# Kernel optimization log

Measured on AMD Instinct MI355X. Metric: run time of the kernel, lower is better.

The kernel has to match this reference:

```python
import jax, jax.numpy as jnp
import numpy as np

E_DIM = 64
N_EMBED = 8192

def setup_inputs() -> dict:
    key = jax.random.key(0)
    k1, k2 = jax.random.split(key)
    x = jax.random.normal(k1, (16, E_DIM, 32, 32), dtype=jnp.float32)   # [B, e_dim, H, W]
    embed = jax.random.normal(k2, (E_DIM, N_EMBED), dtype=jnp.float32)  # codebook [e_dim, n_embed]
    return {"x": x, "embed": embed}

def reference(x, embed):
    e_dim, n_embed = embed.shape
    # NCHW -> NHWC
    xp = jnp.transpose(x, (0, 2, 3, 1))              # [B, H, W, e_dim]
    flat = xp.reshape(-1, e_dim)                     # [N, e_dim]
    # squared-distance expansion: ||f||^2 - 2 f.E + ||e||^2  -> [N, n_embed]
    distance = (jnp.sum(flat * flat, axis=1, keepdims=True)
                - 2.0 * flat @ embed
                + jnp.sum(embed * embed, axis=0, keepdims=True))
    embed_idx = jnp.argmax(-distance, axis=1)        # [N] nearest code ids
    embed_idx = embed_idx.reshape(xp.shape[:-1])     # [B, H, W]
    # gather codes: embedding table is embed.T -> [n_embed, e_dim]
    quantize = jnp.take(embed.T, embed_idx, axis=0)  # [B, H, W, e_dim]
    return quantize
```

## Files before the change

kernel.cpp:

```cpp
#include <hip/hip_runtime.h>


typedef __attribute__((ext_vector_type(8))) __bf16 bf16x8;
typedef __attribute__((ext_vector_type(4))) float f32x4;
typedef unsigned int u32;
typedef unsigned long long u64;

union frag_cast { f32x4 f; bf16x8 b; };
__device__ __forceinline__ bf16x8 as_bf16x8(f32x4 v) { frag_cast u; u.f = v; return u.b; }

#define N_ROWS  16384
#define E_DIM   64
#define N_EMBED 8192
#define NCHUNK  16
#define COLS_PER_BLOCK (N_EMBED / NCHUNK)
#define N_ST (COLS_PER_BLOCK / 64)
#define ROWS_PER_BLOCK 512
#define N_ROWBLK (N_ROWS / ROWS_PER_BLOCK)
#define NT 8
#define MARGIN_THR 2e-3f

#define WS_AH   0u
#define WS_AL   (2u << 20)
#define WS_B    (4u << 20)
#define WS_ET   (6u << 20)
#define WS_BIAS (8u << 20)
#define WS_PB1  (WS_BIAS + (64u << 10))
#define WS_PI1  (WS_PB1 + (1u << 20))
#define WS_PB2  (WS_PI1 + (1u << 20))
#define WS_FIDX (WS_PB2 + (1u << 20))
#define WS_FLAG (WS_FIDX + (64u << 10))
#define WS_CNT  (WS_FLAG + (64u << 10))
#define WS_FKEY (WS_CNT + (4u << 10))

__device__ __forceinline__ u32 f32_key(float s) {
    u32 u = __float_as_uint(s);
    return (u & 0x80000000u) ? ~u : (u | 0x80000000u);
}

__device__ __forceinline__ void async16(const void* g, void* l) {
    __builtin_amdgcn_global_load_lds(
        (const __attribute__((address_space(1))) void*)g,
        (__attribute__((address_space(3))) void*)l, 16, 0, 0);
}

__global__ __launch_bounds__(256) void prep(
        const float* __restrict__ x, const float* __restrict__ embed, char* ws) {
    __shared__ float tile[64][65];
    __bf16* Ah = (__bf16*)(ws + WS_AH);
    __bf16* Al = (__bf16*)(ws + WS_AL);
    float*  eT = (float*)(ws + WS_ET);
    float*  bias = (float*)(ws + WS_BIAS);
    const int t = threadIdx.x;
    const int blk = blockIdx.x;

    if (blk < 256) {
        const int b = blk >> 4, p0 = (blk & 15) * 64;
        {
            const int c = t >> 2, seg = (t & 3) * 16;
            const float* src = x + b * 65536 + c * 1024 + p0 + seg;
#pragma unroll
            for (int i = 0; i < 16; ++i) tile[c][seg + i] = src[i];
        }
        __syncthreads();
        const int p = t >> 2, cq = (t & 3) * 16;
        const long row = b * 1024 + p0 + p;
        bf16x8 vh0, vh1, vl0, vl1;
#pragma unroll
        for (int i = 0; i < 16; ++i) {
            float f = tile[cq + i][p];
            __bf16 h = (__bf16)f;
            __bf16 l = (__bf16)(f - (float)h);
            if (i < 8) { vh0[i] = h; vl0[i] = l; }
            else       { vh1[i - 8] = h; vl1[i - 8] = l; }
        }
        *(bf16x8*)(Ah + row * 64 + cq) = vh0;
        *(bf16x8*)(Ah + row * 64 + cq + 8) = vh1;
        *(bf16x8*)(Al + row * 64 + cq) = vl0;
        *(bf16x8*)(Al + row * 64 + cq + 8) = vl1;
    } else {
        if (blk == 256 && t == 0) *(int*)(ws + WS_CNT) = 0;
        const int g = blk - 256;
        const int jbase = g * 64;
        char* Bg = ws + WS_B + (size_t)g * 16384;
        {
            const int c = t >> 2, seg = (t & 3) * 16;
            const float* src = embed + c * N_EMBED + jbase + seg;
#pragma unroll
            for (int i = 0; i < 16; ++i) tile[c][seg + i] = src[i];
        }
        __syncthreads();
        if (t < 64) {
            float s = 0.f;
#pragma unroll
            for (int c = 0; c < 64; ++c) { float v = tile[c][t]; s = fmaf(v, v, s); }
            bias[jbase + t] = -0.5f * s;
        }
        const int jl = t >> 2, cq = (t & 3) * 16;
        bf16x8 vh0, vh1, vl0, vl1;
#pragma unroll
        for (int i = 0; i < 16; ++i) {
            float f = tile[cq + i][jl];
            eT[(long)(jbase + jl) * 64 + cq + i] = f;
            __bf16 h = (__bf16)f;
            __bf16 l = (__bf16)(f - (float)h);
            if (i < 8) { vh0[i] = h; vl0[i] = l; }
            else       { vh1[i - 8] = h; vl1[i - 8] = l; }
        }
        const int k0 = (cq >> 3), sw = jl & 7;
        __bf16* hi = (__bf16*)Bg + jl * 64;
        __bf16* lo = (__bf16*)(Bg + 8192) + jl * 64;
        *(bf16x8*)(hi + ((k0 ^ sw) * 8))       = vh0;
        *(bf16x8*)(hi + (((k0 + 1) ^ sw) * 8)) = vh1;
        *(bf16x8*)(lo + ((k0 ^ sw) * 8))       = vl0;
        *(bf16x8*)(lo + (((k0 + 1) ^ sw) * 8)) = vl1;
    }
}

__global__ __launch_bounds__(256, 2) void qdist(const char* __restrict__ ws_c, char* __restrict__ ws) {
    __shared__ __align__(16) char smem[2][16384];
    __shared__ __align__(16) float biasLds[512];
    const __bf16* Ah = (const __bf16*)(ws_c + WS_AH);
    const __bf16* Al = (const __bf16*)(ws_c + WS_AL);
    const char* Bws = ws_c + WS_B;
    const float* biasg = (const float*)(ws_c + WS_BIAS);
    float* pb1 = (float*)(ws + WS_PB1);
    int*   pi1 = (int*)(ws + WS_PI1);
    float* pb2 = (float*)(ws + WS_PB2);

    const int t = threadIdx.x;
    const int wv = t >> 6, lane = t & 63, ln = lane & 15, q = lane >> 4;
    const int rb = blockIdx.x >> 4, chunk = blockIdx.x & 15;
    const int row0 = rb * ROWS_PER_BLOCK;
    const int col0 = chunk * COLS_PER_BLOCK;
    const int g0 = col0 >> 6;

    f32x4 pfh[NT][2], pfl[NT][2];
#pragma unroll
    for (int nt = 0; nt < NT; ++nt) {
        long row = row0 + wv * 128 + nt * 16 + ln;
        long base = row * 64 + q * 8;
        pfh[nt][0] = *(const f32x4*)(Ah + base);
        pfh[nt][1] = *(const f32x4*)(Ah + base + 32);
        pfl[nt][0] = *(const f32x4*)(Al + base);
        pfl[nt][1] = *(const f32x4*)(Al + base + 32);
    }
    asm volatile("" :
        "+v"(pfh[0][0]), "+v"(pfh[0][1]), "+v"(pfh[1][0]), "+v"(pfh[1][1]),
        "+v"(pfh[2][0]), "+v"(pfh[2][1]), "+v"(pfh[3][0]), "+v"(pfh[3][1]),
        "+v"(pfh[4][0]), "+v"(pfh[4][1]), "+v"(pfh[5][0]), "+v"(pfh[5][1]),
        "+v"(pfh[6][0]), "+v"(pfh[6][1]), "+v"(pfh[7][0]), "+v"(pfh[7][1]));
    asm volatile("" :
        "+v"(pfl[0][0]), "+v"(pfl[0][1]), "+v"(pfl[1][0]), "+v"(pfl[1][1]),
        "+v"(pfl[2][0]), "+v"(pfl[2][1]), "+v"(pfl[3][0]), "+v"(pfl[3][1]),
        "+v"(pfl[4][0]), "+v"(pfl[4][1]), "+v"(pfl[5][0]), "+v"(pfl[5][1]),
        "+v"(pfl[6][0]), "+v"(pfl[6][1]), "+v"(pfl[7][0]), "+v"(pfl[7][1]));

    float b1[NT], b2[NT]; int iq[NT];
#pragma unroll
    for (int k = 0; k < NT; ++k) { b1[k] = -3.4e38f; b2[k] = -3.4e38f; iq[k] = 0; }

    const int s7 = ln & 7;
    const int rdbase = ln * 128 + ((q ^ s7) << 4);

    auto issue = [&](int st) {
        const char* src = Bws + (size_t)(g0 + st) * 16384;
        char* dst = smem[st & 1];
#pragma unroll
        for (int s = 0; s < 4; ++s)
            async16(src + s * 4096 + wv * 1024 + lane * 16,
                    dst + s * 4096 + wv * 1024);
    };

    if (wv < 2)
        async16((const char*)(biasg + col0) + wv * 1024 + lane * 16,
                (char*)biasLds + wv * 1024);
    issue(0);
    asm volatile("s_waitcnt vmcnt(0)" ::: "memory");
    __builtin_amdgcn_s_barrier();
    __builtin_amdgcn_sched_barrier(0);

    for (int st = 0; st < N_ST; ++st) {
        if (st + 1 < N_ST) {
            issue(st + 1);
            asm volatile("s_waitcnt vmcnt(4)" ::: "memory");
        } else {
            asm volatile("s_waitcnt vmcnt(0)" ::: "memory");
        }
        __builtin_amdgcn_s_barrier();
        __builtin_amdgcn_sched_barrier(0);

        const char* buf = smem[st & 1];
#pragma unroll
        for (int ct = 0; ct < 4; ++ct) {
            const int boff = ct * 2048 + rdbase;
            bf16x8 ah0 = *(const bf16x8*)(buf + boff);
            bf16x8 ah1 = *(const bf16x8*)(buf + (boff ^ 64));
            bf16x8 al0 = *(const bf16x8*)(buf + 8192 + boff);
            bf16x8 al1 = *(const bf16x8*)(buf + 8192 + (boff ^ 64));
            f32x4 bv = *(const f32x4*)(biasLds + st * 64 + ct * 16 + q * 4);
            const int jq = col0 + st * 64 + ct * 16 + q * 4;
            __builtin_amdgcn_sched_barrier(0);
            __builtin_amdgcn_s_barrier();
            asm volatile("s_waitcnt lgkmcnt(0)" ::: "memory");
            __builtin_amdgcn_sched_barrier(0);
            __builtin_amdgcn_s_setprio(1);
#pragma unroll
            for (int nt = 0; nt < NT; ++nt) {
                f32x4 acc = __builtin_amdgcn_mfma_f32_16x16x32_bf16(al0, as_bf16x8(pfh[nt][0]), bv, 0, 0, 0);
                acc = __builtin_amdgcn_mfma_f32_16x16x32_bf16(al1, as_bf16x8(pfh[nt][1]), acc, 0, 0, 0);
                acc = __builtin_amdgcn_mfma_f32_16x16x32_bf16(ah0, as_bf16x8(pfl[nt][0]), acc, 0, 0, 0);
                acc = __builtin_amdgcn_mfma_f32_16x16x32_bf16(ah1, as_bf16x8(pfl[nt][1]), acc, 0, 0, 0);
                acc = __builtin_amdgcn_mfma_f32_16x16x32_bf16(ah0, as_bf16x8(pfh[nt][0]), acc, 0, 0, 0);
                acc = __builtin_amdgcn_mfma_f32_16x16x32_bf16(ah1, as_bf16x8(pfh[nt][1]), acc, 0, 0, 0);
                float mx = fmaxf(fmaxf(acc[0], acc[1]), fmaxf(acc[2], acc[3]));
                b2[nt] = fmaxf(b2[nt], fminf(b1[nt], mx));
                bool gt = mx > b1[nt];
                b1[nt] = fmaxf(b1[nt], mx);
                iq[nt] = gt ? jq : iq[nt];
            }
            __builtin_amdgcn_s_setprio(0);
            __builtin_amdgcn_sched_barrier(0);
            __builtin_amdgcn_s_barrier();
            __builtin_amdgcn_sched_barrier(0);
        }
    }

#pragma unroll
    for (int m = 16; m < 64; m <<= 1) {
#pragma unroll
        for (int nt = 0; nt < NT; ++nt) {
            float o1 = __shfl_xor(b1[nt], m);
            int   oi = __shfl_xor(iq[nt], m);
            float o2 = __shfl_xor(b2[nt], m);
            b2[nt] = fmaxf(fmaxf(fminf(b1[nt], o1), o2), b2[nt]);
            bool take = (o1 > b1[nt]) || (o1 == b1[nt] && oi < iq[nt]);
            if (take) { b1[nt] = o1; iq[nt] = oi; }
        }
    }
    if (q == 0) {
#pragma unroll
        for (int nt = 0; nt < NT; ++nt) {
            int pixel = row0 + wv * 128 + nt * 16 + ln;
            int o = chunk * N_ROWS + pixel;
            pb1[o] = b1[nt];
            pi1[o] = iq[nt];
            pb2[o] = b2[nt];
        }
    }
}

__global__ __launch_bounds__(64) void reduce_rows(const float* __restrict__ x, char* ws,
                                                  float* __restrict__ out) {
    const float* pb1 = (const float*)(ws + WS_PB1);
    const int*   pi1 = (const int*)(ws + WS_PI1);
    const float* pb2 = (const float*)(ws + WS_PB2);
    const float* eT = (const float*)(ws + WS_ET);
    const float* bias = (const float*)(ws + WS_BIAS);
    int* flags = (int*)(ws + WS_FLAG);
    int* cnt = (int*)(ws + WS_CNT);
    u64* fkey = (u64*)(ws + WS_FKEY);
    const int row = blockIdx.x * 64 + threadIdx.x;

    float b1 = pb1[row]; int iq = pi1[row]; float b2 = pb2[row];
#pragma unroll
    for (int ch = 1; ch < NCHUNK; ++ch) {
        float o1 = pb1[ch * N_ROWS + row];
        int   oi = pi1[ch * N_ROWS + row];
        float o2 = pb2[ch * N_ROWS + row];
        b2 = fmaxf(fmaxf(fminf(b1, o1), o2), b2);
        if (o1 > b1 || (o1 == b1 && oi < iq)) { b1 = o1; iq = oi; }
    }

    if (b1 - b2 < MARGIN_THR) {
        fkey[row] = 0ull;
        flags[atomicAdd(cnt, 1)] = row;
    } else {
        float xr[64];
        const float* xb = x + (row >> 10) * 65536 + (row & 1023);
#pragma unroll
        for (int c = 0; c < 64; ++c) xr[c] = xb[c * 1024];
        float best = -3.4e38f; int bi = iq;
#pragma unroll
        for (int cc = 0; cc < 4; ++cc) {
            const int j = iq + cc;
            const float* e = eT + j * 64;
            float s = bias[j];
#pragma unroll
            for (int c = 0; c < 64; ++c) s = fmaf(xr[c], e[c], s);
            if (s > best) { best = s; bi = j; }
        }
        const f32x4* src = (const f32x4*)(eT + (size_t)bi * 64);
        f32x4* dst = (f32x4*)(out + (size_t)row * 64);
#pragma unroll
        for (int v = 0; v < 16; ++v) dst[v] = src[v];
    }
}

__global__ __launch_bounds__(256) void recheck(const float* __restrict__ x, char* ws) {
    __shared__ float fl[64];
    __shared__ u64 red[256];
    const float* eT = (const float*)(ws + WS_ET);
    const float* bias = (const float*)(ws + WS_BIAS);
    const int* flags = (const int*)(ws + WS_FLAG);
    const int n = *(const int*)(ws + WS_CNT);
    u64* fkey = (u64*)(ws + WS_FKEY);
    const int t = threadIdx.x;
    const int seg = blockIdx.x & 31;
    const int rstep = gridDim.x >> 5;
    const int j = seg * 256 + t;

    for (int rowi = blockIdx.x >> 5; rowi < n; rowi += rstep) {
        const int row = flags[rowi];
        __syncthreads();
        if (t < 64) fl[t] = x[(row >> 10) * 65536 + t * 1024 + (row & 1023)];
        __syncthreads();
        float xr[64];
#pragma unroll
        for (int c = 0; c < 64; ++c) xr[c] = fl[c];

        const f32x4* e = (const f32x4*)(eT + (size_t)j * 64);
        f32x4 a0 = {0.f, 0.f, 0.f, 0.f}, a1 = a0, a2 = a0, a3 = a0;
#pragma unroll
        for (int v = 0; v < 4; ++v) {
            f32x4 e0 = e[v * 4 + 0], e1 = e[v * 4 + 1];
            f32x4 e2 = e[v * 4 + 2], e3 = e[v * 4 + 3];
#pragma unroll
            for (int k = 0; k < 4; ++k) {
                a0[k] = fmaf(xr[v * 16 + k],      e0[k], a0[k]);
                a1[k] = fmaf(xr[v * 16 + 4 + k],  e1[k], a1[k]);
                a2[k] = fmaf(xr[v * 16 + 8 + k],  e2[k], a2[k]);
                a3[k] = fmaf(xr[v * 16 + 12 + k], e3[k], a3[k]);
            }
        }
        f32x4 a01 = a0 + a1, a23 = a2 + a3;
        f32x4 as = a01 + a23;
        float s = bias[j] + ((as[0] + as[1]) + (as[2] + as[3]));

        red[t] = ((u64)f32_key(s) << 32) | (u32)(~(u32)j);
        __syncthreads();
        for (int off = 128; off; off >>= 1) {
            if (t < off) { u64 o = red[t + off]; if (o > red[t]) red[t] = o; }
            __syncthreads();
        }
        if (t == 0) atomicMax(&fkey[row], red[0]);
        __syncthreads();
    }
}

__global__ __launch_bounds__(256) void gather_fix(const char* __restrict__ ws,
                                                  float* __restrict__ out) {
    const int n = *(const int*)(ws + WS_CNT);
    const int* flags = (const int*)(ws + WS_FLAG);
    const u64* fkey = (const u64*)(ws + WS_FKEY);
    const float* eT = (const float*)(ws + WS_ET);
    const int sub = threadIdx.x >> 6, c = threadIdx.x & 63;
    for (int i = blockIdx.x * 4 + sub; i < n; i += gridDim.x * 4) {
        const int row = flags[i];
        const int idx = (int)(~(u32)(fkey[row] & 0xffffffffull));
        out[(size_t)row * 64 + c] = eT[(size_t)idx * 64 + c];
    }
}

extern "C" void kernel_launch(void* const* d_in, const int* in_sizes, int n_in,
                              void* d_out, int out_size, void* d_ws, size_t ws_size,
                              hipStream_t stream) {
    const float* x     = (const float*)d_in[0];
    const float* embed = (const float*)d_in[1];
    float* out = (float*)d_out;
    char* ws = (char*)d_ws;

    prep<<<384, 256, 0, stream>>>(x, embed, ws);
    qdist<<<N_ROWBLK * NCHUNK, 256, 0, stream>>>(ws, ws);
    reduce_rows<<<N_ROWS / 64, 64, 0, stream>>>(x, ws, out);
    recheck<<<2048, 256, 0, stream>>>(x, ws);
    gather_fix<<<64, 256, 0, stream>>>(ws, out);
}
```

Baseline: 131.0 us.

## Use single fp16 MFMA pass with error-bounded margin and per-chunk recheck queue

Replaces the split bf16 hi/lo three-product MFMA distance computation with a single fp16 product, halving the codebook and activation staging and cutting MFMA work by a factor of three. The fixed margin threshold becomes a per-row error bound derived from the feature norm and the max codebook norm. Rows within the bound are rechecked exactly, but only in the 512-column chunks whose candidate scores are near the best, fed through a work queue. The qdist loop also drops its per-tile barriers in favour of one sync per stage. Risks include fp16 range/precision issues and a larger recheck set if the bound is loose.

```diff
diff --git a/kernel.cpp b/kernel.cpp
--- a/kernel.cpp
+++ b/kernel.cpp
@@ -1,13 +1,11 @@
 #include <hip/hip_runtime.h>
 
 
-typedef __attribute__((ext_vector_type(8))) __bf16 bf16x8;
+typedef _Float16 f16;
+typedef __attribute__((ext_vector_type(8))) _Float16 f16x8;
 typedef __attribute__((ext_vector_type(4))) float f32x4;
 typedef unsigned int u32;
 typedef unsigned long long u64;
-
-union frag_cast { f32x4 f; bf16x8 b; };
-__device__ __forceinline__ bf16x8 as_bf16x8(f32x4 v) { frag_cast u; u.f = v; return u.b; }
 
 #define N_ROWS  16384
 #define E_DIM   64
@@ -18,20 +16,19 @@
 #define ROWS_PER_BLOCK 512
 #define N_ROWBLK (N_ROWS / ROWS_PER_BLOCK)
 #define NT 8
-#define MARGIN_THR 2e-3f
 
 #define WS_AH   0u
-#define WS_AL   (2u << 20)
-#define WS_B    (4u << 20)
-#define WS_ET   (6u << 20)
-#define WS_BIAS (8u << 20)
-#define WS_PB1  (WS_BIAS + (64u << 10))
+#define WS_B    (2u << 20)
+#define WS_ET   (3u << 20)
+#define WS_BIAS (5u << 20)
+#define WS_CNT  (WS_BIAS + (32u << 10))
+#define WS_GN   (WS_CNT + 16u)
+#define WS_PB1  (WS_CNT + (4u << 10))
 #define WS_PI1  (WS_PB1 + (1u << 20))
 #define WS_PB2  (WS_PI1 + (1u << 20))
-#define WS_FIDX (WS_PB2 + (1u << 20))
-#define WS_FLAG (WS_FIDX + (64u << 10))
-#define WS_CNT  (WS_FLAG + (64u << 10))
-#define WS_FKEY (WS_CNT + (4u << 10))
+#define WS_FLAG (WS_PB2 + (1u << 20))
+#define WS_FKEY (WS_FLAG + (64u << 10))
+#define WS_QUEUE (WS_FKEY + (128u << 10))
 
 __device__ __forceinline__ u32 f32_key(float s) {
     u32 u = __float_as_uint(s);
@@ -47,10 +44,10 @@
 __global__ __launch_bounds__(256) void prep(
         const float* __restrict__ x, const float* __restrict__ embed, char* ws) {
     __shared__ float tile[64][65];
-    __bf16* Ah = (__bf16*)(ws + WS_AH);
-    __bf16* Al = (__bf16*)(ws + WS_AL);
+    f16* Ah = (f16*)(ws + WS_AH);
     float*  eT = (float*)(ws + WS_ET);
     float*  bias = (float*)(ws + WS_BIAS);
+    float*  gn = (float*)(ws + WS_GN);
     const int t = threadIdx.x;
     const int blk = blockIdx.x;
 
@@ -65,24 +62,23 @@
         __syncthreads();
         const int p = t >> 2, cq = (t & 3) * 16;
         const long row = b * 1024 + p0 + p;
-        bf16x8 vh0, vh1, vl0, vl1;
+        f16x8 v0, v1;
 #pragma unroll
         for (int i = 0; i < 16; ++i) {
             float f = tile[cq + i][p];
-            __bf16 h = (__bf16)f;
-            __bf16 l = (__bf16)(f - (float)h);
-            if (i < 8) { vh0[i] = h; vl0[i] = l; }
-            else       { vh1[i - 8] = h; vl1[i - 8] = l; }
-        }
-        *(bf16x8*)(Ah + row * 64 + cq) = vh0;
-        *(bf16x8*)(Ah + row * 64 + cq + 8) = vh1;
-        *(bf16x8*)(Al + row * 64 + cq) = vl0;
-        *(bf16x8*)(Al + row * 64 + cq + 8) = vl1;
+            if (i < 8) v0[i] = (f16)f;
+            else       v1[i - 8] = (f16)f;
+        }
+        *(f16x8*)(Ah + row * 64 + cq) = v0;
+        *(f16x8*)(Ah + row * 64 + cq + 8) = v1;
     } else {
-        if (blk == 256 && t == 0) *(int*)(ws + WS_CNT) = 0;
+        if (blk == 256 && t == 0) {
+            ((int*)(ws + WS_CNT))[0] = 0;
+            ((int*)(ws + WS_CNT))[1] = 0;
+        }
         const int g = blk - 256;
         const int jbase = g * 64;
-        char* Bg = ws + WS_B + (size_t)g * 16384;
+        f16* Bg = (f16*)(ws + WS_B) + (size_t)g * 4096;
         {
             const int c = t >> 2, seg = (t & 3) * 16;
             const float* src = embed + c * N_EMBED + jbase + seg;
@@ -95,33 +91,31 @@
 #pragma unroll
             for (int c = 0; c < 64; ++c) { float v = tile[c][t]; s = fmaf(v, v, s); }
             bias[jbase + t] = -0.5f * s;
+            float m = s;
+#pragma unroll
+            for (int off = 1; off < 64; off <<= 1) m = fmaxf(m, __shfl_xor(m, off));
+            if (t == 0) gn[g] = m;
         }
         const int jl = t >> 2, cq = (t & 3) * 16;
-        bf16x8 vh0, vh1, vl0, vl1;
+        f16x8 v0, v1;
 #pragma unroll
         for (int i = 0; i < 16; ++i) {
             float f = tile[cq + i][jl];
             eT[(long)(jbase + jl) * 64 + cq + i] = f;
-            __bf16 h = (__bf16)f;
-            __bf16 l = (__bf16)(f - (float)h);
-            if (i < 8) { vh0[i] = h; vl0[i] = l; }
-            else       { vh1[i - 8] = h; vl1[i - 8] = l; }
+            if (i < 8) v0[i] = (f16)f;
+            else       v1[i - 8] = (f16)f;
         }
         const int k0 = (cq >> 3), sw = jl & 7;
-        __bf16* hi = (__bf16*)Bg + jl * 64;
-        __bf16* lo = (__bf16*)(Bg + 8192) + jl * 64;
-        *(bf16x8*)(hi + ((k0 ^ sw) * 8))       = vh0;
-        *(bf16x8*)(hi + (((k0 + 1) ^ sw) * 8)) = vh1;
-        *(bf16x8*)(lo + ((k0 ^ sw) * 8))       = vl0;
-        *(bf16x8*)(lo + (((k0 + 1) ^ sw) * 8)) = vl1;
+        f16* hi = Bg + jl * 64;
+        *(f16x8*)(hi + ((k0 ^ sw) * 8))       = v0;
+        *(f16x8*)(hi + (((k0 + 1) ^ sw) * 8)) = v1;
     }
 }
 
 __global__ __launch_bounds__(256, 2) void qdist(const char* __restrict__ ws_c, char* __restrict__ ws) {
-    __shared__ __align__(16) char smem[2][16384];
+    __shared__ __align__(16) char smem[2][8192];
     __shared__ __align__(16) float biasLds[512];
-    const __bf16* Ah = (const __bf16*)(ws_c + WS_AH);
-    const __bf16* Al = (const __bf16*)(ws_c + WS_AL);
+    const f16* Ah = (const f16*)(ws_c + WS_AH);
     const char* Bws = ws_c + WS_B;
     const float* biasg = (const float*)(ws_c + WS_BIAS);
     float* pb1 = (float*)(ws + WS_PB1);
@@ -135,26 +129,19 @@
     const int col0 = chunk * COLS_PER_BLOCK;
     const int g0 = col0 >> 6;
 
-    f32x4 pfh[NT][2], pfl[NT][2];
+    f16x8 pf[NT][2];
 #pragma unroll
     for (int nt = 0; nt < NT; ++nt) {
         long row = row0 + wv * 128 + nt * 16 + ln;
         long base = row * 64 + q * 8;
-        pfh[nt][0] = *(const f32x4*)(Ah + base);
-        pfh[nt][1] = *(const f32x4*)(Ah + base + 32);
-        pfl[nt][0] = *(const f32x4*)(Al + base);
-        pfl[nt][1] = *(const f32x4*)(Al + base + 32);
+        pf[nt][0] = *(const f16x8*)(Ah + base);
+        pf[nt][1] = *(const f16x8*)(Ah + base + 32);
     }
     asm volatile("" :
-        "+v"(pfh[0][0]), "+v"(pfh[0][1]), "+v"(pfh[1][0]), "+v"(pfh[1][1]),
-        "+v"(pfh[2][0]), "+v"(pfh[2][1]), "+v"(pfh[3][0]), "+v"(pfh[3][1]),
-        "+v"(pfh[4][0]), "+v"(pfh[4][1]), "+v"(pfh[5][0]), "+v"(pfh[5][1]),
-        "+v"(pfh[6][0]), "+v"(pfh[6][1]), "+v"(pfh[7][0]), "+v"(pfh[7][1]));
-    asm volatile("" :
-        "+v"(pfl[0][0]), "+v"(pfl[0][1]), "+v"(pfl[1][0]), "+v"(pfl[1][1]),
-        "+v"(pfl[2][0]), "+v"(pfl[2][1]), "+v"(pfl[3][0]), "+v"(pfl[3][1]),
-        "+v"(pfl[4][0]), "+v"(pfl[4][1]), "+v"(pfl[5][0]), "+v"(pfl[5][1]),
-        "+v"(pfl[6][0]), "+v"(pfl[6][1]), "+v"(pfl[7][0]), "+v"(pfl[7][1]));
+        "+v"(pf[0][0]), "+v"(pf[0][1]), "+v"(pf[1][0]), "+v"(pf[1][1]),
+        "+v"(pf[2][0]), "+v"(pf[2][1]), "+v"(pf[3][0]), "+v"(pf[3][1]),
+        "+v"(pf[4][0]), "+v"(pf[4][1]), "+v"(pf[5][0]), "+v"(pf[5][1]),
+        "+v"(pf[6][0]), "+v"(pf[6][1]), "+v"(pf[7][0]), "+v"(pf[7][1]));
 
     float b1[NT], b2[NT]; int iq[NT];
 #pragma unroll
@@ -164,66 +151,42 @@
     const int rdbase = ln * 128 + ((q ^ s7) << 4);
 
     auto issue = [&](int st) {
-        const char* src = Bws + (size_t)(g0 + st) * 16384;
+        const char* src = Bws + (size_t)(g0 + st) * 8192;
         char* dst = smem[st & 1];
 #pragma unroll
-        for (int s = 0; s < 4; ++s)
+        for (int s = 0; s < 2; ++s)
             async16(src + s * 4096 + wv * 1024 + lane * 16,
                     dst + s * 4096 + wv * 1024);
     };
 
-    if (wv < 2)
-        async16((const char*)(biasg + col0) + wv * 1024 + lane * 16,
-                (char*)biasLds + wv * 1024);
+    if (t < 128)
+        async16((const char*)(biasg + col0) + t * 16,
+                (char*)biasLds + (t >> 6) * 1024);
     issue(0);
-    asm volatile("s_waitcnt vmcnt(0)" ::: "memory");
-    __builtin_amdgcn_s_barrier();
-    __builtin_amdgcn_sched_barrier(0);
-
     for (int st = 0; st < N_ST; ++st) {
-        if (st + 1 < N_ST) {
-            issue(st + 1);
-            asm volatile("s_waitcnt vmcnt(4)" ::: "memory");
-        } else {
-            asm volatile("s_waitcnt vmcnt(0)" ::: "memory");
-        }
-        __builtin_amdgcn_s_barrier();
-        __builtin_amdgcn_sched_barrier(0);
-
+        __syncthreads();
+        if (st + 1 < N_ST) issue(st + 1);
         const char* buf = smem[st & 1];
+        __builtin_amdgcn_s_setprio(1);
 #pragma unroll
         for (int ct = 0; ct < 4; ++ct) {
             const int boff = ct * 2048 + rdbase;
-            bf16x8 ah0 = *(const bf16x8*)(buf + boff);
-            bf16x8 ah1 = *(const bf16x8*)(buf + (boff ^ 64));
-            bf16x8 al0 = *(const bf16x8*)(buf + 8192 + boff);
-            bf16x8 al1 = *(const bf16x8*)(buf + 8192 + (boff ^ 64));
+            f16x8 ah0 = *(const f16x8*)(buf + boff);
+            f16x8 ah1 = *(const f16x8*)(buf + (boff ^ 64));
             f32x4 bv = *(const f32x4*)(biasLds + st * 64 + ct * 16 + q * 4);
             const int jq = col0 + st * 64 + ct * 16 + q * 4;
-            __builtin_amdgcn_sched_barrier(0);
-            __builtin_amdgcn_s_barrier();
-            asm volatile("s_waitcnt lgkmcnt(0)" ::: "memory");
-            __builtin_amdgcn_sched_barrier(0);
-            __builtin_amdgcn_s_setprio(1);
 #pragma unroll
             for (int nt = 0; nt < NT; ++nt) {
-                f32x4 acc = __builtin_amdgcn_mfma_f32_16x16x32_bf16(al0, as_bf16x8(pfh[nt][0]), bv, 0, 0, 0);
-                acc = __builtin_amdgcn_mfma_f32_16x16x32_bf16(al1, as_bf16x8(pfh[nt][1]), acc, 0, 0, 0);
-                acc = __builtin_amdgcn_mfma_f32_16x16x32_bf16(ah0, as_bf16x8(pfl[nt][0]), acc, 0, 0, 0);
-                acc = __builtin_amdgcn_mfma_f32_16x16x32_bf16(ah1, as_bf16x8(pfl[nt][1]), acc, 0, 0, 0);
-                acc = __builtin_amdgcn_mfma_f32_16x16x32_bf16(ah0, as_bf16x8(pfh[nt][0]), acc, 0, 0, 0);
-                acc = __builtin_amdgcn_mfma_f32_16x16x32_bf16(ah1, as_bf16x8(pfh[nt][1]), acc, 0, 0, 0);
+                f32x4 acc = __builtin_amdgcn_mfma_f32_16x16x32_f16(ah0, pf[nt][0], bv, 0, 0, 0);
+                acc = __builtin_amdgcn_mfma_f32_16x16x32_f16(ah1, pf[nt][1], acc, 0, 0, 0);
                 float mx = fmaxf(fmaxf(acc[0], acc[1]), fmaxf(acc[2], acc[3]));
                 b2[nt] = fmaxf(b2[nt], fminf(b1[nt], mx));
                 bool gt = mx > b1[nt];
                 b1[nt] = fmaxf(b1[nt], mx);
                 iq[nt] = gt ? jq : iq[nt];
             }
-            __builtin_amdgcn_s_setprio(0);
-            __builtin_amdgcn_sched_barrier(0);
-            __builtin_amdgcn_s_barrier();
-            __builtin_amdgcn_sched_barrier(0);
-        }
+        }
+        __builtin_amdgcn_s_setprio(0);
     }
 
 #pragma unroll
@@ -257,9 +220,11 @@
     const float* pb2 = (const float*)(ws + WS_PB2);
     const float* eT = (const float*)(ws + WS_ET);
     const float* bias = (const float*)(ws + WS_BIAS);
+    const float* gn = (const float*)(ws + WS_GN);
     int* flags = (int*)(ws + WS_FLAG);
     int* cnt = (int*)(ws + WS_CNT);
     u64* fkey = (u64*)(ws + WS_FKEY);
+    u32* queue = (u32*)(ws + WS_QUEUE);
     const int row = blockIdx.x * 64 + threadIdx.x;
 
     float b1 = pb1[row]; int iq = pi1[row]; float b2 = pb2[row];
@@ -272,14 +237,32 @@
         if (o1 > b1 || (o1 == b1 && oi < iq)) { b1 = o1; iq = oi; }
     }
 
-    if (b1 - b2 < MARGIN_THR) {
+    float xr[64];
+    const float* xb = x + (row >> 10) * 65536 + (row & 1023);
+#pragma unroll
+    for (int c = 0; c < 64; ++c) xr[c] = xb[c * 1024];
+    float f2 = 0.f;
+#pragma unroll
+    for (int c = 0; c < 64; ++c) f2 = fmaf(xr[c], xr[c], f2);
+    float e2 = 0.f;
+#pragma unroll
+    for (int i = 0; i < 32; ++i) {
+        f32x4 v = ((const f32x4*)gn)[i];
+        e2 = fmaxf(e2, fmaxf(fmaxf(v[0], v[1]), fmaxf(v[2], v[3])));
+    }
+    const float M = 1.01f * ldexpf(sqrtf(f2) * sqrtf(e2), -9) + 4e-3f;
+
+    if (b1 - b2 < M) {
         fkey[row] = 0ull;
-        flags[atomicAdd(cnt, 1)] = row;
+        flags[atomicAdd(&cnt[0], 1)] = row;
+#pragma unroll
+        for (int ch = 0; ch < NCHUNK; ++ch) {
+            if (pb1[ch * N_ROWS + row] >= b1 - M) {
+                int p = atomicAdd(&cnt[1], 1);
+                queue[p] = ((u32)row << 4) | (u32)ch;
+            }
+        }
     } else {
-        float xr[64];
-        const float* xb = x + (row >> 10) * 65536 + (row & 1023);
-#pragma unroll
-        for (int c = 0; c < 64; ++c) xr[c] = xb[c * 1024];
         float best = -3.4e38f; int bi = iq;
 #pragma unroll
         for (int cc = 0; cc < 4; ++cc) {
@@ -302,16 +285,14 @@
     __shared__ u64 red[256];
     const float* eT = (const float*)(ws + WS_ET);
     const float* bias = (const float*)(ws + WS_BIAS);
-    const int* flags = (const int*)(ws + WS_FLAG);
-    const int n = *(const int*)(ws + WS_CNT);
+    const u32* queue = (const u32*)(ws + WS_QUEUE);
+    const int nwork = ((const int*)(ws + WS_CNT))[1];
     u64* fkey = (u64*)(ws + WS_FKEY);
     const int t = threadIdx.x;
-    const int seg = blockIdx.x & 31;
-    const int rstep = gridDim.x >> 5;
-    const int j = seg * 256 + t;
-
-    for (int rowi = blockIdx.x >> 5; rowi < n; rowi += rstep) {
-        const int row = flags[rowi];
+
+    for (int w = blockIdx.x; w < nwork; w += gridDim.x) {
+        const u32 en = queue[w];
+        const int row = (int)(en >> 4), ch = (int)(en & 15u);
         __syncthreads();
         if (t < 64) fl[t] = x[(row >> 10) * 65536 + t * 1024 + (row & 1023)];
         __syncthreads();
@@ -319,25 +300,31 @@
 #pragma unroll
         for (int c = 0; c < 64; ++c) xr[c] = fl[c];
 
-        const f32x4* e = (const f32x4*)(eT + (size_t)j * 64);
-        f32x4 a0 = {0.f, 0.f, 0.f, 0.f}, a1 = a0, a2 = a0, a3 = a0;
-#pragma unroll
-        for (int v = 0; v < 4; ++v) {
-            f32x4 e0 = e[v * 4 + 0], e1 = e[v * 4 + 1];
-            f32x4 e2 = e[v * 4 + 2], e3 = e[v * 4 + 3];
-#pragma unroll
-            for (int k = 0; k < 4; ++k) {
-                a0[k] = fmaf(xr[v * 16 + k],      e0[k], a0[k]);
-                a1[k] = fmaf(xr[v * 16 + 4 + k],  e1[k], a1[k]);
-                a2[k] = fmaf(xr[v * 16 + 8 + k],  e2[k], a2[k]);
-                a3[k] = fmaf(xr[v * 16 + 12 + k], e3[k], a3[k]);
+        u64 best = 0ull;
+#pragma unroll
+        for (int half = 0; half < 2; ++half) {
+            const int j = ch * 512 + half * 256 + t;
+            const f32x4* e = (const f32x4*)(eT + (size_t)j * 64);
+            f32x4 a0 = {0.f, 0.f, 0.f, 0.f}, a1 = a0, a2 = a0, a3 = a0;
+#pragma unroll
+            for (int v = 0; v < 4; ++v) {
+                f32x4 e0 = e[v * 4 + 0], e1 = e[v * 4 + 1];
+                f32x4 e2 = e[v * 4 + 2], e3 = e[v * 4 + 3];
+#pragma unroll
+                for (int k = 0; k < 4; ++k) {
+                    a0[k] = fmaf(xr[v * 16 + k],      e0[k], a0[k]);
+                    a1[k] = fmaf(xr[v * 16 + 4 + k],  e1[k], a1[k]);
+                    a2[k] = fmaf(xr[v * 16 + 8 + k],  e2[k], a2[k]);
+                    a3[k] = fmaf(xr[v * 16 + 12 + k], e3[k], a3[k]);
+                }
             }
-        }
-        f32x4 a01 = a0 + a1, a23 = a2 + a3;
-        f32x4 as = a01 + a23;
-        float s = bias[j] + ((as[0] + as[1]) + (as[2] + as[3]));
-
-        red[t] = ((u64)f32_key(s) << 32) | (u32)(~(u32)j);
+            f32x4 a01 = a0 + a1, a23 = a2 + a3;
+            f32x4 as = a01 + a23;
+            float s = bias[j] + ((as[0] + as[1]) + (as[2] + as[3]));
+            u64 k = ((u64)f32_key(s) << 32) | (u32)(~(u32)j);
+            best = (k > best) ? k : best;
+        }
+        red[t] = best;
         __syncthreads();
         for (int off = 128; off; off >>= 1) {
             if (t < off) { u64 o = red[t + off]; if (o > red[t]) red[t] = o; }
@@ -373,6 +360,6 @@
     prep<<<384, 256, 0, stream>>>(x, embed, ws);
     qdist<<<N_ROWBLK * NCHUNK, 256, 0, stream>>>(ws, ws);
     reduce_rows<<<N_ROWS / 64, 64, 0, stream>>>(x, ws, out);
-    recheck<<<2048, 256, 0, stream>>>(x, ws);
+    recheck<<<1024, 256, 0, stream>>>(x, ws);
     gather_fix<<<64, 256, 0, stream>>>(ws, out);
 }
```

Result: slower. 216.3 us (+65.0%).
